# Optimization experiments

Measured on AMD Instinct MI355X. Metric: run time of the kernel, lower is better.

The kernel has to match this reference:

```python
import jax, jax.numpy as jnp
import numpy as np

NUM_NODES = 10000
NUM_EDGES = 640000
D_FEAT = 128

def setup_inputs() -> dict:
    key = jax.random.key(0)
    k1, k2 = jax.random.split(key)
    x = jax.random.normal(k1, (NUM_NODES, D_FEAT), dtype=jnp.float32)
    edge_index = jax.random.randint(k2, (2, NUM_EDGES), 0, NUM_NODES, dtype=jnp.int64)
    return {"x": x, "edge_index": edge_index}

def reference(x, edge_index):
    # MessagePassing(aggr='add') with default message/update:
    # msg = x[src]; out[n] = sum of msg over edges with dst == n
    src, dst = edge_index[0], edge_index[1]
    msg = x[src]                                   # [num_edges, d]
    out = jax.ops.segment_sum(msg, dst, num_segments=NUM_NODES)  # [num_nodes, d]
    return out
```

## Files before the change

kernel.cpp:

```cpp
#include <hip/hip_runtime.h>

#define NUM_NODES 10000
#define NUM_EDGES 640000
#define D_FEAT 128

#define BSHIFT 4
#define NPB 16
#define NB 625
#define BLOCKS 256
#define EPB (NUM_EDGES / BLOCKS)
#define CELL_CAP 32
#define MAXB 1344

#define XB_U4 (NUM_NODES * 16)
#define CVT_PER_BLOCK (XB_U4 / BLOCKS)


__device__ __forceinline__ unsigned bf16_rne(float f) {
    unsigned u = __float_as_uint(f);
    return (u + 0x7FFFu + ((u >> 16) & 1u)) >> 16;
}

__global__ __launch_bounds__(256) void scatter_cvt_kernel(
    const int* __restrict__ ei, const float4* __restrict__ x4,
    uint4* __restrict__ xb, unsigned* __restrict__ cnt,
    unsigned* __restrict__ slots) {
    __shared__ int cur[NB];
    int t = threadIdx.x, b = blockIdx.x;
    for (int i = t; i < NB; i += 256) cur[i] = 0;

    int cbase = b * CVT_PER_BLOCK;
    for (int i = t; i < CVT_PER_BLOCK; i += 256) {
        int o = cbase + i;
        float4 a = x4[2 * o];
        float4 c = x4[2 * o + 1];
        uint4 w;
        w.x = bf16_rne(a.x) | (bf16_rne(a.y) << 16);
        w.y = bf16_rne(a.z) | (bf16_rne(a.w) << 16);
        w.z = bf16_rne(c.x) | (bf16_rne(c.y) << 16);
        w.w = bf16_rne(c.z) | (bf16_rne(c.w) << 16);
        xb[o] = w;
    }
    __syncthreads();

    int base = b * EPB;
    for (int j = t; j < EPB; j += 256) {
        int src = ei[base + j];
        int dst = ei[NUM_EDGES + base + j];
        int k = dst >> BSHIFT;
        int pos = atomicAdd(&cur[k], 1);
        if (pos < CELL_CAP)
            slots[(unsigned)(k * BLOCKS + b) * CELL_CAP + (unsigned)pos] =
                ((unsigned)(dst & (NPB - 1)) << 16) | (unsigned)src;
    }
    __syncthreads();
    for (int i = t; i < NB; i += 256)
        cnt[b * NB + i] = (unsigned)min(cur[i], CELL_CAP);
}

__global__ __launch_bounds__(256) void sort_gather_kernel(
    const uint4* __restrict__ xb,
    const unsigned* __restrict__ cnt,
    const uint4* __restrict__ slots4,
    float4* __restrict__ out4)
{
    __shared__ int s_cnt[BLOCKS];
    __shared__ unsigned s_src[MAXB];
    __shared__ int h[NPB];
    __shared__ int off16[NPB];
    __shared__ int cur16[NPB];

    int k = blockIdx.x;
    int t = threadIdx.x;

    if (t < NPB) h[t] = 0;
    s_cnt[t] = (int)cnt[t * NB + k];
    __syncthreads();

    const uint4* sb = slots4 + (unsigned)k * BLOCKS * (CELL_CAP / 4);
    uint4 w4[8];
    int vc[8];
    #pragma unroll
    for (int i = 0; i < 8; ++i) {
        int c = (t >> 3) + 32 * i;
        int sub = t & 7;
        w4[i] = sb[c * 8 + sub];
        int v = s_cnt[c] - sub * 4;
        vc[i] = max(0, min(4, v));
        if (vc[i] > 0) atomicAdd(&h[w4[i].x >> 16], 1);
        if (vc[i] > 1) atomicAdd(&h[w4[i].y >> 16], 1);
        if (vc[i] > 2) atomicAdd(&h[w4[i].z >> 16], 1);
        if (vc[i] > 3) atomicAdd(&h[w4[i].w >> 16], 1);
    }
    __syncthreads();

    if (t == 0) {
        int run = 0;
        for (int m = 0; m < NPB; ++m) { off16[m] = run; cur16[m] = run; run += h[m]; }
    }
    __syncthreads();

    #pragma unroll
    for (int i = 0; i < 8; ++i) {
        if (vc[i] > 0) { int p = atomicAdd(&cur16[w4[i].x >> 16], 1); if (p < MAXB) s_src[p] = w4[i].x & 0xFFFFu; }
        if (vc[i] > 1) { int p = atomicAdd(&cur16[w4[i].y >> 16], 1); if (p < MAXB) s_src[p] = w4[i].y & 0xFFFFu; }
        if (vc[i] > 2) { int p = atomicAdd(&cur16[w4[i].z >> 16], 1); if (p < MAXB) s_src[p] = w4[i].z & 0xFFFFu; }
        if (vc[i] > 3) { int p = atomicAdd(&cur16[w4[i].w >> 16], 1); if (p < MAXB) s_src[p] = w4[i].w & 0xFFFFu; }
    }
    __syncthreads();

    int wave = t >> 6;
    int lane = t & 63;
    int q    = lane >> 4;
    int sub  = lane & 15;

    for (int m = wave; m < NPB; m += 4) {
        int node = k * NPB + m;
        int beg = off16[m];
        int ec  = h[m];
        float a0 = 0.f, a1 = 0.f, a2 = 0.f, a3 = 0.f;
        float a4 = 0.f, a5 = 0.f, a6 = 0.f, a7 = 0.f;
        int j = 0;
        for (; j + 4 <= ec; j += 4) {
            unsigned s = s_src[beg + j + q];
            uint4 w = xb[s * 16u + sub];
            a0 += __uint_as_float(w.x << 16);
            a1 += __uint_as_float(w.x & 0xFFFF0000u);
            a2 += __uint_as_float(w.y << 16);
            a3 += __uint_as_float(w.y & 0xFFFF0000u);
            a4 += __uint_as_float(w.z << 16);
            a5 += __uint_as_float(w.z & 0xFFFF0000u);
            a6 += __uint_as_float(w.w << 16);
            a7 += __uint_as_float(w.w & 0xFFFF0000u);
        }
        if (j + q < ec) {
            unsigned s = s_src[beg + j + q];
            uint4 w = xb[s * 16u + sub];
            a0 += __uint_as_float(w.x << 16);
            a1 += __uint_as_float(w.x & 0xFFFF0000u);
            a2 += __uint_as_float(w.y << 16);
            a3 += __uint_as_float(w.y & 0xFFFF0000u);
            a4 += __uint_as_float(w.z << 16);
            a5 += __uint_as_float(w.z & 0xFFFF0000u);
            a6 += __uint_as_float(w.w << 16);
            a7 += __uint_as_float(w.w & 0xFFFF0000u);
        }
        a0 += __shfl_down(a0, 32); a1 += __shfl_down(a1, 32);
        a2 += __shfl_down(a2, 32); a3 += __shfl_down(a3, 32);
        a4 += __shfl_down(a4, 32); a5 += __shfl_down(a5, 32);
        a6 += __shfl_down(a6, 32); a7 += __shfl_down(a7, 32);
        a0 += __shfl_down(a0, 16); a1 += __shfl_down(a1, 16);
        a2 += __shfl_down(a2, 16); a3 += __shfl_down(a3, 16);
        a4 += __shfl_down(a4, 16); a5 += __shfl_down(a5, 16);
        a6 += __shfl_down(a6, 16); a7 += __shfl_down(a7, 16);
        if (q == 0) {
            unsigned o = (unsigned)node * 32u + (unsigned)sub * 2u;
            out4[o]     = make_float4(a0, a1, a2, a3);
            out4[o + 1] = make_float4(a4, a5, a6, a7);
        }
    }
}

extern "C" void kernel_launch(void* const* d_in, const int* in_sizes, int n_in,
                              void* d_out, int out_size, void* d_ws, size_t ws_size,
                              hipStream_t stream) {
    const float* x   = (const float*)d_in[0];
    const int*   ei  = (const int*)d_in[1];
    float*       out = (float*)d_out;

    uint4*    xb    = (uint4*)d_ws;
    unsigned* cnt   = (unsigned*)(xb + XB_U4);
    unsigned* slots = cnt + BLOCKS * NB;

    scatter_cvt_kernel<<<BLOCKS, 256, 0, stream>>>(
        ei, (const float4*)x, xb, cnt, slots);

    sort_gather_kernel<<<NB, 256, 0, stream>>>(
        xb, cnt, (const uint4*)slots, (float4*)out);
}
```

Baseline: 90.30 us.

## Fuse scatter and gather into one cooperative kernel with LDS-staged buckets

Merges the scatter/convert kernel and the sort/gather kernel into a single cooperative launch of 625 blocks, separated by a grid-wide sync. This removes the second launch and the gap between kernels. Each block now bins its 1024 edges into per-bucket cells in shared memory and writes them out in one coalesced pass. The cell capacity drops to 16 and the bucket matrix becomes 625x625. The gather phase then does more strided reads of counts and slots, adds grid-sync overhead, and requires all 625 blocks to be co-resident.

```diff
diff --git a/kernel.cpp b/kernel.cpp
--- a/kernel.cpp
+++ b/kernel.cpp
@@ -1,4 +1,7 @@
 #include <hip/hip_runtime.h>
+#include <hip/hip_cooperative_groups.h>
+
+namespace cg = cooperative_groups;
 
 #define NUM_NODES 10000
 #define NUM_EDGES 640000
@@ -7,31 +10,40 @@
 #define BSHIFT 4
 #define NPB 16
 #define NB 625
-#define BLOCKS 256
-#define EPB (NUM_EDGES / BLOCKS)
-#define CELL_CAP 32
+#define EPB (NUM_EDGES / NB)
+#define CELL_CAP 16
+#define CELL_U4 (CELL_CAP / 4)
 #define MAXB 1344
 
 #define XB_U4 (NUM_NODES * 16)
-#define CVT_PER_BLOCK (XB_U4 / BLOCKS)
 
+#define CNT_PAD (((NB * NB) + 3) & ~3)
 
 __device__ __forceinline__ unsigned bf16_rne(float f) {
     unsigned u = __float_as_uint(f);
     return (u + 0x7FFFu + ((u >> 16) & 1u)) >> 16;
 }
 
-__global__ __launch_bounds__(256) void scatter_cvt_kernel(
+__global__ __launch_bounds__(256) void fused_kernel(
     const int* __restrict__ ei, const float4* __restrict__ x4,
     uint4* __restrict__ xb, unsigned* __restrict__ cnt,
-    unsigned* __restrict__ slots) {
+    uint4* __restrict__ slots4, float4* __restrict__ out4) {
     __shared__ int cur[NB];
-    int t = threadIdx.x, b = blockIdx.x;
+    __shared__ unsigned stage[NB * CELL_CAP];
+    __shared__ int s_cnt[NB];
+    __shared__ unsigned s_src[MAXB];
+    __shared__ int h[NPB];
+    __shared__ int off16[NPB];
+    __shared__ int cur16[NPB];
+
+    cg::grid_group grid = cg::this_grid();
+    int t = threadIdx.x;
+    int b = blockIdx.x;
+
     for (int i = t; i < NB; i += 256) cur[i] = 0;
 
-    int cbase = b * CVT_PER_BLOCK;
-    for (int i = t; i < CVT_PER_BLOCK; i += 256) {
-        int o = cbase + i;
+    {
+        int o = b * 256 + t;
         float4 a = x4[2 * o];
         float4 c = x4[2 * o + 1];
         uint4 w;
@@ -43,54 +55,56 @@
     }
     __syncthreads();
 
-    int base = b * EPB;
-    for (int j = t; j < EPB; j += 256) {
-        int src = ei[base + j];
-        int dst = ei[NUM_EDGES + base + j];
-        int k = dst >> BSHIFT;
-        int pos = atomicAdd(&cur[k], 1);
-        if (pos < CELL_CAP)
-            slots[(unsigned)(k * BLOCKS + b) * CELL_CAP + (unsigned)pos] =
-                ((unsigned)(dst & (NPB - 1)) << 16) | (unsigned)src;
+    {
+        int base = b * EPB;
+        #pragma unroll
+        for (int r = 0; r < EPB / 256; ++r) {
+            int j = base + r * 256 + t;
+            int src = ei[j];
+            int dst = ei[NUM_EDGES + j];
+            int k = dst >> BSHIFT;
+            int pos = atomicAdd(&cur[k], 1);
+            if (pos < CELL_CAP)
+                stage[k * CELL_CAP + pos] =
+                    ((unsigned)(dst & (NPB - 1)) << 16) | (unsigned)src;
+        }
     }
     __syncthreads();
-    for (int i = t; i < NB; i += 256)
-        cnt[b * NB + i] = (unsigned)min(cur[i], CELL_CAP);
-}
 
-__global__ __launch_bounds__(256) void sort_gather_kernel(
-    const uint4* __restrict__ xb,
-    const unsigned* __restrict__ cnt,
-    const uint4* __restrict__ slots4,
-    float4* __restrict__ out4)
-{
-    __shared__ int s_cnt[BLOCKS];
-    __shared__ unsigned s_src[MAXB];
-    __shared__ int h[NPB];
-    __shared__ int off16[NPB];
-    __shared__ int cur16[NPB];
+    {
+        const uint4* st4 = (const uint4*)stage;
+        uint4* dst4 = slots4 + (unsigned)b * (NB * CELL_U4);
+        for (int i = t; i < NB * CELL_U4; i += 256) dst4[i] = st4[i];
+        for (int i = t; i < NB; i += 256)
+            cnt[b * NB + i] = (unsigned)min(cur[i], CELL_CAP);
+    }
 
-    int k = blockIdx.x;
-    int t = threadIdx.x;
+    __threadfence();
+    grid.sync();
+
+    int k = b;
 
     if (t < NPB) h[t] = 0;
-    s_cnt[t] = (int)cnt[t * NB + k];
+    for (int i = t; i < NB; i += 256) s_cnt[i] = (int)cnt[i * NB + k];
     __syncthreads();
 
-    const uint4* sb = slots4 + (unsigned)k * BLOCKS * (CELL_CAP / 4);
-    uint4 w4[8];
-    int vc[8];
+    uint4 w4[10];
+    int vc[10];
     #pragma unroll
-    for (int i = 0; i < 8; ++i) {
-        int c = (t >> 3) + 32 * i;
-        int sub = t & 7;
-        w4[i] = sb[c * 8 + sub];
-        int v = s_cnt[c] - sub * 4;
-        vc[i] = max(0, min(4, v));
-        if (vc[i] > 0) atomicAdd(&h[w4[i].x >> 16], 1);
-        if (vc[i] > 1) atomicAdd(&h[w4[i].y >> 16], 1);
-        if (vc[i] > 2) atomicAdd(&h[w4[i].z >> 16], 1);
-        if (vc[i] > 3) atomicAdd(&h[w4[i].w >> 16], 1);
+    for (int i = 0; i < 10; ++i) {
+        int j = t + 256 * i;
+        vc[i] = 0;
+        if (j < NB * CELL_U4) {
+            int c   = j >> 2;
+            int sub = j & 3;
+            w4[i] = slots4[((unsigned)c * NB + k) * CELL_U4 + sub];
+            int v = s_cnt[c] - sub * 4;
+            vc[i] = max(0, min(4, v));
+            if (vc[i] > 0) atomicAdd(&h[w4[i].x >> 16], 1);
+            if (vc[i] > 1) atomicAdd(&h[w4[i].y >> 16], 1);
+            if (vc[i] > 2) atomicAdd(&h[w4[i].z >> 16], 1);
+            if (vc[i] > 3) atomicAdd(&h[w4[i].w >> 16], 1);
+        }
     }
     __syncthreads();
 
@@ -101,7 +115,7 @@
     __syncthreads();
 
     #pragma unroll
-    for (int i = 0; i < 8; ++i) {
+    for (int i = 0; i < 10; ++i) {
         if (vc[i] > 0) { int p = atomicAdd(&cur16[w4[i].x >> 16], 1); if (p < MAXB) s_src[p] = w4[i].x & 0xFFFFu; }
         if (vc[i] > 1) { int p = atomicAdd(&cur16[w4[i].y >> 16], 1); if (p < MAXB) s_src[p] = w4[i].y & 0xFFFFu; }
         if (vc[i] > 2) { int p = atomicAdd(&cur16[w4[i].z >> 16], 1); if (p < MAXB) s_src[p] = w4[i].z & 0xFFFFu; }
@@ -164,17 +178,16 @@
 extern "C" void kernel_launch(void* const* d_in, const int* in_sizes, int n_in,
                               void* d_out, int out_size, void* d_ws, size_t ws_size,
                               hipStream_t stream) {
-    const float* x   = (const float*)d_in[0];
-    const int*   ei  = (const int*)d_in[1];
-    float*       out = (float*)d_out;
+    const int*    ei  = (const int*)d_in[1];
+    const float4* x4  = (const float4*)d_in[0];
+    float4*       out = (float4*)d_out;
 
-    uint4*    xb    = (uint4*)d_ws;
-    unsigned* cnt   = (unsigned*)(xb + XB_U4);
-    unsigned* slots = cnt + BLOCKS * NB;
+    uint4*    xb     = (uint4*)d_ws;
+    unsigned* cnt    = (unsigned*)(xb + XB_U4);
+    uint4*    slots4 = (uint4*)(cnt + CNT_PAD);
 
-    scatter_cvt_kernel<<<BLOCKS, 256, 0, stream>>>(
-        ei, (const float4*)x, xb, cnt, slots);
-
-    sort_gather_kernel<<<NB, 256, 0, stream>>>(
-        xb, cnt, (const uint4*)slots, (float4*)out);
+    void* args[] = { (void*)&ei, (void*)&x4, (void*)&xb, (void*)&cnt,
+                     (void*)&slots4, (void*)&out };
+    hipLaunchCooperativeKernel((void*)fused_kernel, dim3(NB), dim3(256),
+                               args, 0, stream);
 }
```

Measured after the change: 231.6 us. 2.57x slower.

## Bucket edges into coarse 256-node regions with LDS-staged coalesced segment writes

Applied to the files above, without the earlier changes.

The producer kernel now bins edges into 40 coarse regions of 256 nodes, stages them in shared memory and writes fixed-width segments with coalesced stores, instead of scattering 4-byte slot writes across 625 fine buckets. Each gather block reads its whole region's segments and keeps only edges belonging to its 16 nodes, building per-node source lists directly. This replaces the histogram/prefix/sort step in the old gather kernel. The cost is that every region is re-read by 16 blocks, roughly four times more index traffic in total, plus filtering work. New per-segment and per-node caps could drop edges if the degree distribution is skewed.

```diff
diff --git a/kernel.cpp b/kernel.cpp
--- a/kernel.cpp
+++ b/kernel.cpp
@@ -4,16 +4,18 @@
 #define NUM_EDGES 640000
 #define D_FEAT 128
 
-#define BSHIFT 4
 #define NPB 16
 #define NB 625
-#define BLOCKS 256
-#define EPB (NUM_EDGES / BLOCKS)
-#define CELL_CAP 32
-#define MAXB 1344
+#define REG 40
+#define PRODB 256
+#define EPB (NUM_EDGES / PRODB)
+#define SEG_W 128
+#define SEG_PAD 129
+#define NODE_CAP 160
+#define LIST_PAD 161
 
 #define XB_U4 (NUM_NODES * 16)
-#define CVT_PER_BLOCK (XB_U4 / BLOCKS)
+#define CVT_PER_B (XB_U4 / PRODB)
 
 
 __device__ __forceinline__ unsigned bf16_rne(float f) {
@@ -24,14 +26,15 @@
 __global__ __launch_bounds__(256) void scatter_cvt_kernel(
     const int* __restrict__ ei, const float4* __restrict__ x4,
     uint4* __restrict__ xb, unsigned* __restrict__ cnt,
-    unsigned* __restrict__ slots) {
-    __shared__ int cur[NB];
+    unsigned* __restrict__ segs)
+{
+    __shared__ int cur[REG];
+    __shared__ unsigned stage[REG * SEG_PAD];
     int t = threadIdx.x, b = blockIdx.x;
-    for (int i = t; i < NB; i += 256) cur[i] = 0;
+    if (t < REG) cur[t] = 0;
 
-    int cbase = b * CVT_PER_BLOCK;
-    for (int i = t; i < CVT_PER_BLOCK; i += 256) {
-        int o = cbase + i;
+    for (int i = t; i < CVT_PER_B; i += 256) {
+        int o = b * CVT_PER_B + i;
         float4 a = x4[2 * o];
         float4 c = x4[2 * o + 1];
         uint4 w;
@@ -47,65 +50,49 @@
     for (int j = t; j < EPB; j += 256) {
         int src = ei[base + j];
         int dst = ei[NUM_EDGES + base + j];
-        int k = dst >> BSHIFT;
-        int pos = atomicAdd(&cur[k], 1);
-        if (pos < CELL_CAP)
-            slots[(unsigned)(k * BLOCKS + b) * CELL_CAP + (unsigned)pos] =
-                ((unsigned)(dst & (NPB - 1)) << 16) | (unsigned)src;
-    }
-    __syncthreads();
-    for (int i = t; i < NB; i += 256)
-        cnt[b * NB + i] = (unsigned)min(cur[i], CELL_CAP);
-}
-
-__global__ __launch_bounds__(256) void sort_gather_kernel(
-    const uint4* __restrict__ xb,
-    const unsigned* __restrict__ cnt,
-    const uint4* __restrict__ slots4,
-    float4* __restrict__ out4)
-{
-    __shared__ int s_cnt[BLOCKS];
-    __shared__ unsigned s_src[MAXB];
-    __shared__ int h[NPB];
-    __shared__ int off16[NPB];
-    __shared__ int cur16[NPB];
-
-    int k = blockIdx.x;
-    int t = threadIdx.x;
-
-    if (t < NPB) h[t] = 0;
-    s_cnt[t] = (int)cnt[t * NB + k];
-    __syncthreads();
-
-    const uint4* sb = slots4 + (unsigned)k * BLOCKS * (CELL_CAP / 4);
-    uint4 w4[8];
-    int vc[8];
-    #pragma unroll
-    for (int i = 0; i < 8; ++i) {
-        int c = (t >> 3) + 32 * i;
-        int sub = t & 7;
-        w4[i] = sb[c * 8 + sub];
-        int v = s_cnt[c] - sub * 4;
-        vc[i] = max(0, min(4, v));
-        if (vc[i] > 0) atomicAdd(&h[w4[i].x >> 16], 1);
-        if (vc[i] > 1) atomicAdd(&h[w4[i].y >> 16], 1);
-        if (vc[i] > 2) atomicAdd(&h[w4[i].z >> 16], 1);
-        if (vc[i] > 3) atomicAdd(&h[w4[i].w >> 16], 1);
+        int r = dst >> 8;
+        int pos = atomicAdd(&cur[r], 1);
+        if (pos < SEG_W)
+            stage[r * SEG_PAD + pos] =
+                ((unsigned)(dst & 255) << 16) | (unsigned)src;
     }
     __syncthreads();
 
-    if (t == 0) {
-        int run = 0;
-        for (int m = 0; m < NPB; ++m) { off16[m] = run; cur16[m] = run; run += h[m]; }
+    for (int i = t; i < REG * SEG_W; i += 256) {
+        int r = i >> 7, w = i & (SEG_W - 1);
+        segs[((unsigned)r * PRODB + b) * SEG_W + w] = stage[r * SEG_PAD + w];
     }
+    if (t < REG) cnt[t * PRODB + b] = (unsigned)min(cur[t], SEG_W);
+}
+
+__global__ __launch_bounds__(256) void gather_kernel(
+    const uint4* __restrict__ xb,
+    const unsigned* __restrict__ cnt,
+    const uint4* __restrict__ segs4,
+    float4* __restrict__ out4)
+{
+    __shared__ int s_cnt[PRODB];
+    __shared__ int cur16[NPB];
+    __shared__ unsigned s_list[NPB * LIST_PAD];
+    int k = blockIdx.x, t = threadIdx.x;
+    int r = k >> 4;
+    unsigned kb = (unsigned)(k & 15);
+
+    s_cnt[t] = (int)cnt[r * PRODB + t];
+    if (t < NPB) cur16[t] = 0;
     __syncthreads();
 
-    #pragma unroll
-    for (int i = 0; i < 8; ++i) {
-        if (vc[i] > 0) { int p = atomicAdd(&cur16[w4[i].x >> 16], 1); if (p < MAXB) s_src[p] = w4[i].x & 0xFFFFu; }
-        if (vc[i] > 1) { int p = atomicAdd(&cur16[w4[i].y >> 16], 1); if (p < MAXB) s_src[p] = w4[i].y & 0xFFFFu; }
-        if (vc[i] > 2) { int p = atomicAdd(&cur16[w4[i].z >> 16], 1); if (p < MAXB) s_src[p] = w4[i].z & 0xFFFFu; }
-        if (vc[i] > 3) { int p = atomicAdd(&cur16[w4[i].w >> 16], 1); if (p < MAXB) s_src[p] = w4[i].w & 0xFFFFu; }
+    const uint4* rb = segs4 + (unsigned)r * (PRODB * SEG_W / 4);
+    #pragma unroll 4
+    for (int i = 0; i < 32; ++i) {
+        int j4 = t + 256 * i;
+        uint4 w = rb[j4];
+        int n  = s_cnt[j4 >> 5];
+        int bw = (j4 & 31) * 4;
+        if (bw + 0 < n && (w.x >> 20) == kb) { int p = atomicAdd(&cur16[(w.x >> 16) & 15], 1); if (p < NODE_CAP) s_list[((w.x >> 16) & 15) * LIST_PAD + p] = w.x & 0xFFFFu; }
+        if (bw + 1 < n && (w.y >> 20) == kb) { int p = atomicAdd(&cur16[(w.y >> 16) & 15], 1); if (p < NODE_CAP) s_list[((w.y >> 16) & 15) * LIST_PAD + p] = w.y & 0xFFFFu; }
+        if (bw + 2 < n && (w.z >> 20) == kb) { int p = atomicAdd(&cur16[(w.z >> 16) & 15], 1); if (p < NODE_CAP) s_list[((w.z >> 16) & 15) * LIST_PAD + p] = w.z & 0xFFFFu; }
+        if (bw + 3 < n && (w.w >> 20) == kb) { int p = atomicAdd(&cur16[(w.w >> 16) & 15], 1); if (p < NODE_CAP) s_list[((w.w >> 16) & 15) * LIST_PAD + p] = w.w & 0xFFFFu; }
     }
     __syncthreads();
 
@@ -116,13 +103,13 @@
 
     for (int m = wave; m < NPB; m += 4) {
         int node = k * NPB + m;
-        int beg = off16[m];
-        int ec  = h[m];
+        int ec = min(cur16[m], NODE_CAP);
+        const unsigned* lst = s_list + m * LIST_PAD;
         float a0 = 0.f, a1 = 0.f, a2 = 0.f, a3 = 0.f;
         float a4 = 0.f, a5 = 0.f, a6 = 0.f, a7 = 0.f;
         int j = 0;
         for (; j + 4 <= ec; j += 4) {
-            unsigned s = s_src[beg + j + q];
+            unsigned s = lst[j + q];
             uint4 w = xb[s * 16u + sub];
             a0 += __uint_as_float(w.x << 16);
             a1 += __uint_as_float(w.x & 0xFFFF0000u);
@@ -134,7 +121,7 @@
             a7 += __uint_as_float(w.w & 0xFFFF0000u);
         }
         if (j + q < ec) {
-            unsigned s = s_src[beg + j + q];
+            unsigned s = lst[j + q];
             uint4 w = xb[s * 16u + sub];
             a0 += __uint_as_float(w.x << 16);
             a1 += __uint_as_float(w.x & 0xFFFF0000u);
@@ -164,17 +151,16 @@
 extern "C" void kernel_launch(void* const* d_in, const int* in_sizes, int n_in,
                               void* d_out, int out_size, void* d_ws, size_t ws_size,
                               hipStream_t stream) {
-    const float* x   = (const float*)d_in[0];
-    const int*   ei  = (const int*)d_in[1];
-    float*       out = (float*)d_out;
+    const float4* x4  = (const float4*)d_in[0];
+    const int*    ei  = (const int*)d_in[1];
+    float4*       out = (float4*)d_out;
 
-    uint4*    xb    = (uint4*)d_ws;
-    unsigned* cnt   = (unsigned*)(xb + XB_U4);
-    unsigned* slots = cnt + BLOCKS * NB;
+    uint4*    xb   = (uint4*)d_ws;
+    unsigned* cnt  = (unsigned*)(xb + XB_U4);
+    unsigned* segs = cnt + REG * PRODB;
 
-    scatter_cvt_kernel<<<BLOCKS, 256, 0, stream>>>(
-        ei, (const float4*)x, xb, cnt, slots);
+    scatter_cvt_kernel<<<PRODB, 256, 0, stream>>>(ei, x4, xb, cnt, segs);
 
-    sort_gather_kernel<<<NB, 256, 0, stream>>>(
-        xb, cnt, (const uint4*)slots, (float4*)out);
+    gather_kernel<<<NB, 256, 0, stream>>>(
+        xb, cnt, (const uint4*)segs, out);
 }
```

Result: slower. 109.4 us (+21.1%).
